# Kernel tuning notes

Measured on AMD Instinct MI355X. Metric: run time of the kernel, lower is better.

Reference implementation:

```python
import jax, jax.numpy as jnp
import numpy as np

B = 4; D = H = W = 28; C = 192; NH = 6; WS = 7; SS = 3
L = D * H * W; N = WS ** 3; HD = C // NH


def _rel_index():
    c = np.stack(np.meshgrid(np.arange(WS), np.arange(WS), np.arange(WS), indexing='ij')).reshape(3, -1)
    r = c[:, :, None] - c[:, None, :] + (WS - 1)
    return jnp.asarray(r[0] * (2 * WS - 1) ** 2 + r[1] * (2 * WS - 1) + r[2])  # (N,N)


def _attn_mask():
    img = np.zeros((D, H, W), np.float32)
    sl = (slice(0, -WS), slice(-WS, -SS), slice(-SS, None))
    cnt = 0
    for d in sl:
        for h in sl:
            for w in sl:
                img[d, h, w] = cnt; cnt += 1
    mw = img.reshape(D // WS, WS, H // WS, WS, W // WS, WS).transpose(0, 2, 4, 1, 3, 5).reshape(-1, N)
    am = mw[:, None, :] - mw[:, :, None]
    return jnp.asarray(np.where(am != 0, -100.0, 0.0).astype(np.float32))  # (nW,N,N)

REL_IDX = _rel_index()
ATTN_MASK = _attn_mask()


def _ln(x, g, b):
    m = x.mean(-1, keepdims=True)
    v = ((x - m) ** 2).mean(-1, keepdims=True)
    return (x - m) / jnp.sqrt(v + 1e-5) * g + b


def _window_partition(x):  # (B,D,H,W,C) -> (B*nW, N, C)
    x = x.reshape(B, D // WS, WS, H // WS, WS, W // WS, WS, C)
    return x.transpose(0, 1, 3, 5, 2, 4, 6, 7).reshape(-1, N, C)


def _window_reverse(w):  # (B*nW, N, C) -> (B,D,H,W,C)
    x = w.reshape(B, D // WS, H // WS, W // WS, WS, WS, WS, C)
    return x.transpose(0, 1, 4, 2, 5, 3, 6, 7).reshape(B, D, H, W, C)


def setup_inputs() -> dict:
    key = jax.random.key(0)
    ks = jax.random.split(key, 8)
    s = 0.02
    return {
        'x': jax.random.normal(ks[0], (B, L, C), jnp.float32),
        'norm1_g': jnp.ones((C,), jnp.float32), 'norm1_b': jnp.zeros((C,), jnp.float32),
        'qkv_w': jax.random.normal(ks[1], (3 * C, C), jnp.float32) * s,
        'qkv_b': jnp.zeros((3 * C,), jnp.float32),
        'proj_w': jax.random.normal(ks[2], (C, C), jnp.float32) * s,
        'proj_b': jnp.zeros((C,), jnp.float32),
        'rel_table': jax.random.normal(ks[3], ((2 * WS - 1) ** 3, NH), jnp.float32) * s,
        'norm2_g': jnp.ones((C,), jnp.float32), 'norm2_b': jnp.zeros((C,), jnp.float32),
        'fc1_w': jax.random.normal(ks[4], (4 * C, C), jnp.float32) * s,
        'fc1_b': jnp.zeros((4 * C,), jnp.float32),
        'fc2_w': jax.random.normal(ks[5], (C, 4 * C), jnp.float32) * s,
        'fc2_b': jnp.zeros((C,), jnp.float32),
    }


def reference(x, norm1_g, norm1_b, qkv_w, qkv_b, proj_w, proj_b, rel_table,
              norm2_g, norm2_b, fc1_w, fc1_b, fc2_w, fc2_b):
    shortcut = x
    h = _ln(x, norm1_g, norm1_b).reshape(B, D, H, W, C)
    h = jnp.roll(h, (-SS, -SS, -SS), axis=(1, 2, 3))
    xw = _window_partition(h)                                  # (B_, N, C)
    B_ = xw.shape[0]
    qkv = (xw @ qkv_w.T + qkv_b).reshape(B_, N, 3, NH, HD).transpose(2, 0, 3, 1, 4)
    q, k, v = qkv[0], qkv[1], qkv[2]                           # (B_, NH, N, HD)
    attn = jnp.einsum('bhnd,bhmd->bhnm', q * (HD ** -0.5), k)
    bias = rel_table[REL_IDX].transpose(2, 0, 1)               # (NH, N, N)
    attn = attn + bias[None]
    nW = ATTN_MASK.shape[0]
    attn = (attn.reshape(B, nW, NH, N, N) + ATTN_MASK[None, :, None]).reshape(B_, NH, N, N)
    attn = jax.nn.softmax(attn, axis=-1)
    out = jnp.einsum('bhnm,bhmd->bhnd', attn, v).transpose(0, 2, 1, 3).reshape(B_, N, C)
    out = out @ proj_w.T + proj_b
    h = _window_reverse(out)
    h = jnp.roll(h, (SS, SS, SS), axis=(1, 2, 3)).reshape(B, L, C)
    x = shortcut + h
    y = _ln(x, norm2_g, norm2_b)
    y = jax.nn.gelu(y @ fc1_w.T + fc1_b, approximate=False)
    return x + (y @ fc2_w.T + fc2_b)
```

## Files before the change

### kernel.cpp

```cpp
#include <hip/hip_runtime.h>

#define DEV __device__ __forceinline__

typedef __bf16 bf16x8 __attribute__((ext_vector_type(8)));
typedef float f32x4 __attribute__((ext_vector_type(4)));

DEV float bflo(unsigned int u) { union { unsigned int x; float f; } c; c.x = u << 16; return c.f; }
DEV unsigned short f2bf(float f) {
  union { float f; unsigned int u; } c; c.f = f;
  unsigned int u = c.u;
  return (unsigned short)((u + 0x7fffu + ((u >> 16) & 1u)) >> 16);
}
DEV unsigned int pkbf(float a, float b) {
  unsigned int r;
  asm("v_cvt_pk_bf16_f32 %0, %1, %2" : "=v"(r) : "v"(a), "v"(b));
  return r;
}
DEV float gelu_fast(float y) {
  float y2 = y * y;
  float z = y * fmaf(y2, 0.10294348f, 2.30220842f);
  float e = __builtin_amdgcn_exp2f(z);
  float r = __builtin_amdgcn_rcpf(e + 1.0f);
  return fmaf(-y, r, y);
}

DEV void gload16(const void* g, void* l) {
  __builtin_amdgcn_global_load_lds((const __attribute__((address_space(1))) void*)g,
                                   (__attribute__((address_space(3))) void*)l, 16, 0, 0);
}

__global__ __launch_bounds__(256) void wconv_all(const float* __restrict__ s0,
                                                 const float* __restrict__ s1,
                                                 const float* __restrict__ s2,
                                                 const float* __restrict__ s3,
                                                 unsigned short* __restrict__ dst) {
  int i = blockIdx.x * 256 + threadIdx.x;
  const float* src; int off, real;
  if (i < 122880)      { src = s0; off = i;          real = 110592; }
  else if (i < 172032) { src = s1; off = i - 122880; real = 36864; }
  else if (i < 319488) { src = s2; off = i - 172032; real = 147456; }
  else                 { src = s3; off = i - 319488; real = 147456; }
  dst[i] = (off < real) ? f2bf(src[off]) : (unsigned short)0;
}

__global__ __launch_bounds__(256) void bmt_kernel(const float* __restrict__ rel_table,
                                                  unsigned short* __restrict__ bmt4) {
  int wth = blockIdx.x;
  int wt = wth / 6, h = wth - wt * 6;
  int r = blockIdx.y;
  unsigned short* row = bmt4 + (((size_t)wth * 88 + r) * 352) * 4;
  for (int q = threadIdx.x; q < 352; q += 256) {
    int mb_q = 0, cls_q = 0;
    bool qv = q < 343;
    if (qv) {
      int ii_q = q / 49, rem_q = q - ii_q * 49;
      int jj_q = rem_q / 7, ww_q = rem_q - jj_q * 7;
      mb_q = ii_q * 169 + jj_q * 13 + ww_q;
      int cd_q = (wt & 4) ? (ii_q < 4 ? 1 : 2) : 0;
      int ch_q = (wt & 2) ? (jj_q < 4 ? 1 : 2) : 0;
      int cw_q = (wt & 1) ? (ww_q < 4 ? 1 : 2) : 0;
      cls_q = cd_q * 9 + ch_q * 3 + cw_q;
    }
    unsigned short ov[4];
#pragma unroll
    for (int i = 0; i < 4; i++) {
      int kk = 4 * r + i;
      float v;
      if (kk >= 343) v = -30000.f;
      else if (!qv) v = 0.f;
      else {
        int ii_k = kk / 49, rem_k = kk - ii_k * 49;
        int jj_k = rem_k / 7, ww_k = rem_k - jj_k * 7;
        int mb_k = ii_k * 169 + jj_k * 13 + ww_k;
        int cd_k = (wt & 4) ? (ii_k < 4 ? 1 : 2) : 0;
        int ch_k = (wt & 2) ? (jj_k < 4 ? 1 : 2) : 0;
        int cw_k = (wt & 1) ? (ww_k < 4 ? 1 : 2) : 0;
        int cls_k = cd_k * 9 + ch_k * 3 + cw_k;
        v = rel_table[(mb_q - mb_k + 1098) * 6 + h] * 1.4426950408889634f;
        if (cls_q != cls_k) v -= 144.26950408889634f;
      }
      ov[i] = f2bf(v);
    }
    unsigned int lo = (unsigned)ov[0] | ((unsigned)ov[1] << 16);
    unsigned int hi = (unsigned)ov[2] | ((unsigned)ov[3] << 16);
    *(uint2*)(row + q * 4) = make_uint2(lo, hi);
  }
}

__global__ __launch_bounds__(256) void ln_kernel(const float* __restrict__ x,
                                                 const float* __restrict__ g,
                                                 const float* __restrict__ b,
                                                 unsigned short* __restrict__ out) {
  int row = (blockIdx.x << 2) + (threadIdx.x >> 6);
  int lane = threadIdx.x & 63;
  int w_ = row / 343, n_ = row - w_ * 343;
  int bb = w_ >> 6, wrem = w_ & 63;
  int wd = wrem >> 4, wh = (wrem >> 2) & 3, ww = wrem & 3;
  int ii = n_ / 49, rem = n_ - ii * 49;
  int jj = rem / 7, kk = rem - jj * 7;
  int d = wd * 7 + ii + 3; if (d >= 28) d -= 28;
  int hh = wh * 7 + jj + 3; if (hh >= 28) hh -= 28;
  int wb = ww * 7 + kk + 3; if (wb >= 28) wb -= 28;
  const float* xr = x + ((size_t)bb * 21952 + (d * 28 + hh) * 28 + wb) * 192;
  float v0 = xr[lane], v1 = xr[lane + 64], v2 = xr[lane + 128];
  float s = v0 + v1 + v2;
  float sq = v0 * v0 + v1 * v1 + v2 * v2;
#pragma unroll
  for (int o = 32; o > 0; o >>= 1) {
    s += __shfl_xor(s, o, 64);
    sq += __shfl_xor(sq, o, 64);
  }
  float mean = s * (1.0f / 192.0f);
  float var = sq * (1.0f / 192.0f) - mean * mean;
  float rstd = rsqrtf(var + 1e-5f);
  unsigned short* orow = out + (size_t)row * 192;
  orow[lane]       = f2bf((v0 - mean) * rstd * g[lane] + b[lane]);
  orow[lane + 64]  = f2bf((v1 - mean) * rstd * g[lane + 64] + b[lane + 64]);
  orow[lane + 128] = f2bf((v2 - mean) * rstd * g[lane + 128] + b[lane + 128]);
}

__global__ __launch_bounds__(256) void gemm_qkv(
    const unsigned short* __restrict__ A, const unsigned short* __restrict__ W,
    const float* __restrict__ bias,
    unsigned short* __restrict__ oq, unsigned short* __restrict__ okk,
    unsigned short* __restrict__ ov) {
  __shared__ __align__(16) unsigned short As[2][128 * 32];
  __shared__ __align__(16) unsigned short Bs[2][128 * 32];
  const int K = 192;
  const int orig = blockIdx.x;
  const int xcd = orig & 7, off = orig >> 3;
  const int wgid = (xcd < 6 ? xcd * 429 : 2574 + (xcd - 6) * 428) + off;
  const int by = wgid / 5, bx = wgid - by * 5;
  const int bm = by << 7, bn = bx << 7;

  const int tid = threadIdx.x;
  const int lane = tid & 63;
  const int wv = tid >> 6;
  const int wr = wv >> 1, wc = wv & 1;
  const int l15 = lane & 15, l4 = lane >> 4;

  f32x4 acc[4][4];
#pragma unroll
  for (int a = 0; a < 4; a++)
#pragma unroll
    for (int b2 = 0; b2 < 4; b2++) acc[a][b2] = (f32x4){0.f, 0.f, 0.f, 0.f};

  auto stage = [&](int kt, int buf) {
#pragma unroll
    for (int i = 0; i < 2; i++) {
      int o = (i << 12) + (tid << 4);
      int r = o >> 6;
      int c = (o >> 4) & 3;
      int sc = (c ^ (r & 3)) << 3;
      gload16(A + (size_t)(bm + r) * K + kt * 32 + sc, &As[buf][o >> 1]);
      gload16(W + (size_t)(bn + r) * K + kt * 32 + sc, &Bs[buf][o >> 1]);
    }
  };

  stage(0, 0);
  int cur = 0;
  for (int kt = 0; kt < 6; ++kt) {
    if (kt < 5) {
      stage(kt + 1, cur ^ 1);
      asm volatile("s_waitcnt vmcnt(4)" ::: "memory");
    } else {
      asm volatile("s_waitcnt vmcnt(0)" ::: "memory");
    }
    __builtin_amdgcn_s_barrier();
    __builtin_amdgcn_sched_barrier(0);
    {
      bf16x8 af[4], bfr[4];
#pragma unroll
      for (int fm = 0; fm < 4; fm++) {
        int r = (wr << 6) + (fm << 4) + l15;
        af[fm] = *(const bf16x8*)(&As[cur][(r << 5) + ((l4 ^ (r & 3)) << 3)]);
      }
#pragma unroll
      for (int fn = 0; fn < 4; fn++) {
        int r = (wc << 6) + (fn << 4) + l15;
        bfr[fn] = *(const bf16x8*)(&Bs[cur][(r << 5) + ((l4 ^ (r & 3)) << 3)]);
      }
#pragma unroll
      for (int fm = 0; fm < 4; fm++)
#pragma unroll
        for (int fn = 0; fn < 4; fn++)
          acc[fm][fn] = __builtin_amdgcn_mfma_f32_16x16x32_bf16(bfr[fn], af[fm], acc[fm][fn], 0, 0, 0);
    }
    if (kt < 5) {
      __builtin_amdgcn_sched_barrier(0);
      __builtin_amdgcn_s_barrier();
      cur ^= 1;
    }
  }

#pragma unroll
  for (int fm = 0; fm < 4; fm++) {
    int gr = bm + (wr << 6) + (fm << 4) + l15;
    int w_ = gr / 343, n_ = gr - w_ * 343;
#pragma unroll
    for (int fn = 0; fn < 4; fn++) {
      int gc0 = bn + (wc << 6) + (fn << 4) + (l4 << 2);
      if (gc0 < 576) {
        float4 bv = *(const float4*)(bias + gc0);
        float v0 = acc[fm][fn][0] + bv.x, v1 = acc[fm][fn][1] + bv.y;
        float v2 = acc[fm][fn][2] + bv.z, v3 = acc[fm][fn][3] + bv.w;
        int which = gc0 / 192;
        int cc3 = gc0 - which * 192;
        int hh2 = cc3 >> 5, dd0 = cc3 & 31;
        size_t offo = ((size_t)(w_ * 6 + hh2) * 343 + n_) * 32 + dd0;
        if (which == 0) {
          const float sc = 0.17677669529663687f * 1.4426950408889634f;
          *(uint2*)(oq + offo) = make_uint2(pkbf(v0 * sc, v1 * sc), pkbf(v2 * sc, v3 * sc));
        } else if (which == 1) {
          *(uint2*)(okk + offo) = make_uint2(pkbf(v0, v1), pkbf(v2, v3));
        } else {
          *(uint2*)(ov + offo) = make_uint2(pkbf(v0, v1), pkbf(v2, v3));
        }
      }
    }
  }
}

__global__ __launch_bounds__(256, 2) void proj_mlp(
    const unsigned short* __restrict__ A,
    const unsigned short* __restrict__ Wp, const float* __restrict__ bp,
    const float* __restrict__ x,
    const float* __restrict__ g2, const float* __restrict__ b2,
    const unsigned short* __restrict__ W1, const float* __restrict__ b1,
    const unsigned short* __restrict__ W2, const float* __restrict__ b2b,
    float* __restrict__ out) {
  __shared__ __align__(16) char smem[41984];
  unsigned short* As = (unsigned short*)smem;
  unsigned short* Hs = (unsigned short*)(smem + 24576);
  float* red = (float*)(smem + 24576);

  const int tid = threadIdx.x, lane = tid & 63, wv = tid >> 6;
  const int l15 = lane & 15, l4 = lane >> 4;
  const int bm = blockIdx.x << 6;

  int orow[4];
#pragma unroll
  for (int fm = 0; fm < 4; fm++) {
    int gr = bm + (fm << 4) + l15;
    int w_ = gr / 343, n_ = gr - w_ * 343;
    int bb = w_ >> 6, wrem = w_ & 63;
    int wd = wrem >> 4, wh = (wrem >> 2) & 3, ww = wrem & 3;
    int ii = n_ / 49, rem = n_ - ii * 49;
    int jj = rem / 7, kk = rem - jj * 7;
    int d = wd * 7 + ii + 3; if (d >= 28) d -= 28;
    int hh = wh * 7 + jj + 3; if (hh >= 28) hh -= 28;
    int wb = ww * 7 + kk + 3; if (wb >= 28) wb -= 28;
    orow[fm] = ((bb * 21952 + (d * 28 + hh) * 28 + wb) * 192);
  }

#pragma unroll
  for (int i = 0; i < 6; i++) {
    int idx = (i << 8) + tid;
    int r = idx / 24, c = idx - r * 24;
    gload16(A + (size_t)(bm + r) * 192 + ((c ^ (r & 7)) << 3), As + r * 192 + (c << 3));
  }
  asm volatile("s_waitcnt vmcnt(0)" ::: "memory");
  __builtin_amdgcn_s_barrier();

  f32x4 acc[4][3];
#pragma unroll
  for (int a = 0; a < 4; a++)
#pragma unroll
    for (int b_ = 0; b_ < 3; b_++) acc[a][b_] = (f32x4){0.f, 0.f, 0.f, 0.f};
  __builtin_amdgcn_s_setprio(1);
#pragma unroll
  for (int ks = 0; ks < 6; ks++) {
    bf16x8 af[4], wpf[3];
#pragma unroll
    for (int fm = 0; fm < 4; fm++) {
      int r = (fm << 4) + l15;
      int ch = (ks << 2) + l4;
      af[fm] = *(const bf16x8*)(As + r * 192 + ((ch ^ (r & 7)) << 3));
    }
#pragma unroll
    for (int fn = 0; fn < 3; fn++) {
      int rr = wv * 48 + (fn << 4) + l15;
      wpf[fn] = *(const bf16x8*)(Wp + (size_t)rr * 192 + (ks << 5) + (l4 << 3));
    }
#pragma unroll
    for (int fm = 0; fm < 4; fm++)
#pragma unroll
      for (int fn = 0; fn < 3; fn++)
        acc[fm][fn] = __builtin_amdgcn_mfma_f32_16x16x32_bf16(wpf[fn], af[fm], acc[fm][fn], 0, 0, 0);
  }
  __builtin_amdgcn_s_setprio(0);

  float ps[4], psq[4];
#pragma unroll
  for (int fm = 0; fm < 4; fm++) {
    float s = 0.f, sq = 0.f;
#pragma unroll
    for (int fn = 0; fn < 3; fn++) {
      int gc0 = wv * 48 + (fn << 4) + (l4 << 2);
      float4 bv = *(const float4*)(bp + gc0);
      float4 xv = *(const float4*)(x + (size_t)orow[fm] + gc0);
      acc[fm][fn][0] += bv.x + xv.x;
      acc[fm][fn][1] += bv.y + xv.y;
      acc[fm][fn][2] += bv.z + xv.z;
      acc[fm][fn][3] += bv.w + xv.w;
#pragma unroll
      for (int i = 0; i < 4; i++) {
        float v = acc[fm][fn][i];
        s += v; sq += v * v;
      }
    }
    ps[fm] = s; psq[fm] = sq;
  }
#pragma unroll
  for (int fm = 0; fm < 4; fm++) {
    ps[fm] += __shfl_xor(ps[fm], 16, 64);
    ps[fm] += __shfl_xor(ps[fm], 32, 64);
    psq[fm] += __shfl_xor(psq[fm], 16, 64);
    psq[fm] += __shfl_xor(psq[fm], 32, 64);
  }
  __syncthreads();
  if (l4 == 0) {
#pragma unroll
    for (int fm = 0; fm < 4; fm++) {
      int tr = (fm << 4) + l15;
      red[tr * 8 + wv] = ps[fm];
      red[tr * 8 + 4 + wv] = psq[fm];
    }
  }
  __syncthreads();
  if (tid < 64) {
    float s = red[tid * 8] + red[tid * 8 + 1] + red[tid * 8 + 2] + red[tid * 8 + 3];
    float sq = red[tid * 8 + 4] + red[tid * 8 + 5] + red[tid * 8 + 6] + red[tid * 8 + 7];
    float mean = s * (1.0f / 192.0f);
    float var = sq * (1.0f / 192.0f) - mean * mean;
    red[tid * 8] = mean;
    red[tid * 8 + 1] = rsqrtf(var + 1e-5f);
  }
  __syncthreads();
  unsigned int xnb[4][3][2];
#pragma unroll
  for (int fm = 0; fm < 4; fm++) {
    int tr = (fm << 4) + l15;
    float mean = red[tr * 8], rstd = red[tr * 8 + 1];
#pragma unroll
    for (int fn = 0; fn < 3; fn++) {
      int gc0 = wv * 48 + (fn << 4) + (l4 << 2);
      float4 gv = *(const float4*)(g2 + gc0);
      float4 b2v = *(const float4*)(b2 + gc0);
      float v0 = acc[fm][fn][0], v1 = acc[fm][fn][1];
      float v2 = acc[fm][fn][2], v3 = acc[fm][fn][3];
      xnb[fm][fn][0] = pkbf(v0, v1);
      xnb[fm][fn][1] = pkbf(v2, v3);
      float y0 = (v0 - mean) * rstd * gv.x + b2v.x;
      float y1 = (v1 - mean) * rstd * gv.y + b2v.y;
      float y2 = (v2 - mean) * rstd * gv.z + b2v.z;
      float y3 = (v3 - mean) * rstd * gv.w + b2v.w;
      int ch = gc0 >> 3;
      *(uint2*)(As + tr * 192 + ((ch ^ (tr & 7)) << 3) + (gc0 & 7)) =
          make_uint2(pkbf(y0, y1), pkbf(y2, y3));
    }
  }
  __syncthreads();

  f32x4 acc2[4][3];
#pragma unroll
  for (int a = 0; a < 4; a++)
#pragma unroll
    for (int b_ = 0; b_ < 3; b_++) acc2[a][b_] = (f32x4){0.f, 0.f, 0.f, 0.f};

#pragma unroll
  for (int cc = 0; cc < 6; cc++) {
    bf16x8 w1f[2][6];
#pragma unroll
    for (int fn = 0; fn < 2; fn++)
#pragma unroll
      for (int ks = 0; ks < 6; ks++) {
        int hrow = (cc << 7) + (wv << 5) + (fn << 4) + l15;
        w1f[fn][ks] = *(const bf16x8*)(W1 + (size_t)hrow * 192 + (ks << 5) + (l4 << 3));
      }
    bf16x8 w2f[3][4];
#pragma unroll
    for (int fn = 0; fn < 3; fn++)
#pragma unroll
      for (int ks = 0; ks < 4; ks++) {
        int j = wv * 48 + (fn << 4) + l15;
        w2f[fn][ks] = *(const bf16x8*)(W2 + (size_t)j * 768 + (cc << 7) + (ks << 5) + (l4 << 3));
      }
    f32x4 acc1[4][2];
#pragma unroll
    for (int a = 0; a < 4; a++) {
      acc1[a][0] = (f32x4){0.f, 0.f, 0.f, 0.f};
      acc1[a][1] = (f32x4){0.f, 0.f, 0.f, 0.f};
    }
    __builtin_amdgcn_s_setprio(1);
#pragma unroll
    for (int ks = 0; ks < 6; ks++) {
      bf16x8 af[4];
#pragma unroll
      for (int fm = 0; fm < 4; fm++) {
        int r = (fm << 4) + l15;
        int ch = (ks << 2) + l4;
        af[fm] = *(const bf16x8*)(As + r * 192 + ((ch ^ (r & 7)) << 3));
      }
#pragma unroll
      for (int fm = 0; fm < 4; fm++)
#pragma unroll
        for (int fn = 0; fn < 2; fn++)
          acc1[fm][fn] = __builtin_amdgcn_mfma_f32_16x16x32_bf16(w1f[fn][ks], af[fm], acc1[fm][fn], 0, 0, 0);
    }
    __builtin_amdgcn_s_setprio(0);
    __syncthreads();
#pragma unroll
    for (int fm = 0; fm < 4; fm++) {
      int r = (fm << 4) + l15;
#pragma unroll
      for (int fn = 0; fn < 2; fn++) {
        int hc = (wv << 5) + (fn << 4) + (l4 << 2);
        float4 bv = *(const float4*)(b1 + (cc << 7) + hc);
        float g0 = gelu_fast(acc1[fm][fn][0] + bv.x);
        float g1 = gelu_fast(acc1[fm][fn][1] + bv.y);
        float g2_ = gelu_fast(acc1[fm][fn][2] + bv.z);
        float g3 = gelu_fast(acc1[fm][fn][3] + bv.w);
        *(uint2*)(Hs + r * 136 + hc) = make_uint2(pkbf(g0, g1), pkbf(g2_, g3));
      }
    }
    __syncthreads();
    __builtin_amdgcn_s_setprio(1);
#pragma unroll
    for (int ks = 0; ks < 4; ks++) {
      bf16x8 hf[4];
#pragma unroll
      for (int fm = 0; fm < 4; fm++) {
        int r = (fm << 4) + l15;
        hf[fm] = *(const bf16x8*)(Hs + r * 136 + (ks << 5) + (l4 << 3));
      }
#pragma unroll
      for (int fm = 0; fm < 4; fm++)
#pragma unroll
        for (int fn = 0; fn < 3; fn++)
          acc2[fm][fn] = __builtin_amdgcn_mfma_f32_16x16x32_bf16(w2f[fn][ks], hf[fm], acc2[fm][fn], 0, 0, 0);
    }
    __builtin_amdgcn_s_setprio(0);
  }

#pragma unroll
  for (int fm = 0; fm < 4; fm++) {
#pragma unroll
    for (int fn = 0; fn < 3; fn++) {
      int gc0 = wv * 48 + (fn << 4) + (l4 << 2);
      float4 bv = *(const float4*)(b2b + gc0);
      float4 o;
      o.x = acc2[fm][fn][0] + bv.x + bflo(xnb[fm][fn][0] & 0xffffu);
      o.y = acc2[fm][fn][1] + bv.y + bflo(xnb[fm][fn][0] >> 16);
      o.z = acc2[fm][fn][2] + bv.z + bflo(xnb[fm][fn][1] & 0xffffu);
      o.w = acc2[fm][fn][3] + bv.w + bflo(xnb[fm][fn][1] >> 16);
      *(float4*)(out + (size_t)orow[fm] + gc0) = o;
    }
  }
}

__global__ __launch_bounds__(256) void attn_mfma(const unsigned short* __restrict__ q,
                                                 const unsigned short* __restrict__ k,
                                                 const unsigned short* __restrict__ v,
                                                 const unsigned short* __restrict__ bmt4,
                                                 unsigned short* __restrict__ out) {
  __shared__ __align__(16) unsigned short Ks[352 * 32];
  __shared__ __align__(16) unsigned short Vt[32 * 360];

  const int blk = blockIdx.x;
  const int h_ = blk >> 8;
  const int idx = blk & 255;
  const int cums[8] = {0, 108, 144, 180, 192, 228, 240, 252};
  int c = (idx >= 108) + (idx >= 144) + (idx >= 180) + (idx >= 192) +
          (idx >= 228) + (idx >= 240) + (idx >= 252);
  int r0 = idx - cums[c];
  int sh = (c & 2) ? 1 : 3, sw = (c & 1) ? 1 : 3;
  int p = ((c & 4) ? 1 : 3) * sh * sw;
  int b = r0 / p, q2 = r0 - b * p;
  int wd, wh, ww;
  if (c & 4) wd = 3; else { wd = q2 / (sh * sw); q2 -= wd * sh * sw; }
  if (c & 2) wh = 3; else { wh = q2 / sw; q2 -= wh * sw; }
  ww = (c & 1) ? 3 : q2;
  const int w_ = b * 64 + wd * 16 + wh * 4 + ww;
  const int wt = c;
  const int blkqkv = w_ * 6 + h_;

  const int t = threadIdx.x, lane = t & 63, wv = t >> 6;
  const int l15 = lane & 15, l4 = lane >> 4;
  const unsigned short* Qb = q + (size_t)blkqkv * (343 * 32);
  const unsigned short* Kb = k + (size_t)blkqkv * (343 * 32);
  const unsigned short* Vb = v + (size_t)blkqkv * (343 * 32);
  const unsigned short* bm4 = bmt4 + ((size_t)(wt * 6 + h_) * 88) * 352 * 4;

  for (int cc = t; cc < 1408; cc += 256) {
    int r = cc >> 2, ch = cc & 3;
    int swc = ch ^ ((r >> 1) & 3);
    uint4 val = make_uint4(0, 0, 0, 0);
    if (r < 343) val = *(const uint4*)(Kb + r * 32 + ch * 8);
    *(uint4*)(Ks + r * 32 + swc * 8) = val;
  }
#pragma unroll
  for (int ch = 0; ch < 4; ch++) {
    for (int n = t; n < 343; n += 256) {
      union { uint4 u4; unsigned short us[8]; } val;
      val.u4 = *(const uint4*)(Vb + n * 32 + ch * 8);
#pragma unroll
      for (int j = 0; j < 8; j++) Vt[(ch * 8 + j) * 360 + n] = val.us[j];
    }
  }
  for (int cc = t; cc < 288; cc += 256) {
    int d = cc / 9, n = 343 + (cc - d * 9);
    Vt[d * 360 + n] = 0;
  }
  __syncthreads();

  const int ksw = (l4 ^ ((l15 >> 1) & 3)) << 3;

  for (int tq = wv; tq < 22; tq += 4) {
    int qrow = tq * 16 + l15; if (qrow > 342) qrow = 342;
    bf16x8 qf = *(const bf16x8*)(Qb + qrow * 32 + l4 * 8);

    unsigned int u0[22], u1[22];
    float lsum = 0.f;
    __builtin_amdgcn_s_setprio(1);
#pragma unroll
    for (int kt = 0; kt < 22; kt++) {
      bf16x8 kf = *(const bf16x8*)(Ks + (kt * 16 + l15) * 32 + ksw);
      f32x4 s = __builtin_amdgcn_mfma_f32_16x16x32_bf16(kf, qf, (f32x4){0.f, 0.f, 0.f, 0.f}, 0, 0, 0);
      const unsigned short* bp = bm4 + ((size_t)((kt << 2) + l4) * 352 + (tq << 4) + l15) * 4;
      uint2 bv = *(const uint2*)bp;
      float p0 = __builtin_amdgcn_exp2f(s[0] + bflo(bv.x & 0xffffu));
      float p1 = __builtin_amdgcn_exp2f(s[1] + bflo(bv.x >> 16));
      float p2 = __builtin_amdgcn_exp2f(s[2] + bflo(bv.y & 0xffffu));
      float p3 = __builtin_amdgcn_exp2f(s[3] + bflo(bv.y >> 16));
      lsum += (p0 + p1) + (p2 + p3);
      asm("v_cvt_pk_bf16_f32 %0, %1, %2" : "=v"(u0[kt]) : "v"(p0), "v"(p1));
      asm("v_cvt_pk_bf16_f32 %0, %1, %2" : "=v"(u1[kt]) : "v"(p2), "v"(p3));
    }
    __builtin_amdgcn_s_setprio(0);
    lsum += __shfl_xor(lsum, 16, 64);
    lsum += __shfl_xor(lsum, 32, 64);
    float inv = 1.0f / lsum;

    f32x4 oacc0 = (f32x4){0.f, 0.f, 0.f, 0.f};
    f32x4 oacc1 = (f32x4){0.f, 0.f, 0.f, 0.f};
    __builtin_amdgcn_s_setprio(1);
#pragma unroll
    for (int ck = 0; ck < 11; ck++) {
      unsigned int dw[4];
#pragma unroll
      for (int d = 0; d < 4; d++) {
        int src = l15 + 16 * ((d >> 1) + 2 * (l4 & 1));
        unsigned int x = __shfl((d & 1) ? u1[2 * ck] : u0[2 * ck], src, 64);
        unsigned int y = __shfl((d & 1) ? u1[2 * ck + 1] : u0[2 * ck + 1], src, 64);
        dw[d] = (l4 < 2) ? x : y;
      }
      union { unsigned int u[4]; bf16x8 v; } pc;
      pc.u[0] = dw[0]; pc.u[1] = dw[1]; pc.u[2] = dw[2]; pc.u[3] = dw[3];
      bf16x8 vf0 = *(const bf16x8*)(Vt + (size_t)l15 * 360 + ck * 32 + l4 * 8);
      bf16x8 vf1 = *(const bf16x8*)(Vt + (size_t)(16 + l15) * 360 + ck * 32 + l4 * 8);
      oacc0 = __builtin_amdgcn_mfma_f32_16x16x32_bf16(vf0, pc.v, oacc0, 0, 0, 0);
      oacc1 = __builtin_amdgcn_mfma_f32_16x16x32_bf16(vf1, pc.v, oacc1, 0, 0, 0);
    }
    __builtin_amdgcn_s_setprio(0);

    int qg = tq * 16 + l15;
    if (qg < 343) {
      unsigned short* orow = out + ((size_t)w_ * 343 + qg) * 192 + h_ * 32;
      *(uint2*)(orow + (l4 << 2)) =
          make_uint2(pkbf(oacc0[0] * inv, oacc0[1] * inv), pkbf(oacc0[2] * inv, oacc0[3] * inv));
      *(uint2*)(orow + 16 + (l4 << 2)) =
          make_uint2(pkbf(oacc1[0] * inv, oacc1[1] * inv), pkbf(oacc1[2] * inv, oacc1[3] * inv));
    }
  }
}

extern "C" void kernel_launch(void* const* d_in, const int* in_sizes, int n_in,
                              void* d_out, int out_size, void* d_ws, size_t ws_size,
                              hipStream_t stream) {
  const float* x      = (const float*)d_in[0];
  const float* n1g    = (const float*)d_in[1];
  const float* n1b    = (const float*)d_in[2];
  const float* qkv_w  = (const float*)d_in[3];
  const float* qkv_b  = (const float*)d_in[4];
  const float* proj_w = (const float*)d_in[5];
  const float* proj_b = (const float*)d_in[6];
  const float* rel_t  = (const float*)d_in[7];
  const float* n2g    = (const float*)d_in[8];
  const float* n2b    = (const float*)d_in[9];
  const float* fc1_w  = (const float*)d_in[10];
  const float* fc1_b  = (const float*)d_in[11];
  const float* fc2_w  = (const float*)d_in[12];
  const float* fc2_b  = (const float*)d_in[13];

  char* ws = (char*)d_ws;
  if (ws_size < 147820032ull) return;
  unsigned short* WQKV  = (unsigned short*)(ws);
  unsigned short* WPROJ = (unsigned short*)(ws + 245760);
  unsigned short* WFC1  = (unsigned short*)(ws + 344064);
  unsigned short* WFC2  = (unsigned short*)(ws + 638976);
  unsigned short* XW    = (unsigned short*)(ws + 1032192);
  unsigned short* Q_    = (unsigned short*)(ws + 34750464);
  unsigned short* K_    = (unsigned short*)(ws + 68468736);
  unsigned short* V_    = (unsigned short*)(ws + 102187008);
  unsigned short* BMT4  = (unsigned short*)(ws + 135925248);
  float* OUT = (float*)d_out;

  wconv_all<<<2016, 256, 0, stream>>>(qkv_w, proj_w, fc1_w, fc2_w, WQKV);

  bmt_kernel<<<dim3(48, 88), 256, 0, stream>>>(rel_t, BMT4);

  ln_kernel<<<21952, 256, 0, stream>>>(x, n1g, n1b, XW);

  gemm_qkv<<<3430, 256, 0, stream>>>(XW, WQKV, qkv_b, Q_, K_, V_);

  attn_mfma<<<1536, 256, 0, stream>>>(Q_, K_, V_, BMT4, XW);

  proj_mlp<<<1372, 256, 0, stream>>>(XW, WPROJ, proj_b, x, n2g, n2b,
                                     WFC1, fc1_b, WFC2, fc2_b, OUT);
}
```

Baseline: 324.1 us.

## Widen proj_mlp blocks to 128 rows with double-buffered GELU tile

The fused proj+LN+MLP kernel now uses 512-thread blocks that cover 128 rows, in two row groups of four waves. Each weight fragment the kernel loads therefore feeds twice as many rows, halving the block count. The hidden (GELU) tile is double-buffered so the barrier before writing it can be dropped, and the W2 fragment loads move after the fc1 MFMAs to shorten their live range. The s_setprio hints are removed. In exchange, LDS per block rises to about 116 KB, which likely allows only one block per CU, and the tighter register budget may cause spills or lower occupancy.

```diff
diff --git a/kernel.cpp b/kernel.cpp
--- a/kernel.cpp
+++ b/kernel.cpp
@@ -221,7 +221,7 @@
   }
 }
 
-__global__ __launch_bounds__(256, 2) void proj_mlp(
+__global__ __launch_bounds__(512, 2) void proj_mlp(
     const unsigned short* __restrict__ A,
     const unsigned short* __restrict__ Wp, const float* __restrict__ bp,
     const float* __restrict__ x,
@@ -229,19 +229,21 @@
     const unsigned short* __restrict__ W1, const float* __restrict__ b1,
     const unsigned short* __restrict__ W2, const float* __restrict__ b2b,
     float* __restrict__ out) {
-  __shared__ __align__(16) char smem[41984];
-  unsigned short* As = (unsigned short*)smem;
-  unsigned short* Hs = (unsigned short*)(smem + 24576);
-  float* red = (float*)(smem + 24576);
+  __shared__ __align__(16) char smem[118784];
+  unsigned short* As  = (unsigned short*)smem;
+  unsigned short* Hs0 = (unsigned short*)(smem + 49152);
+  unsigned short* Hs1 = (unsigned short*)(smem + 83968);
+  float* red = (float*)(smem + 49152);
 
   const int tid = threadIdx.x, lane = tid & 63, wv = tid >> 6;
+  const int wq = wv & 3, rg = wv >> 2;
   const int l15 = lane & 15, l4 = lane >> 4;
-  const int bm = blockIdx.x << 6;
+  const int bm = blockIdx.x << 7;
 
   int orow[4];
 #pragma unroll
   for (int fm = 0; fm < 4; fm++) {
-    int gr = bm + (fm << 4) + l15;
+    int gr = bm + (rg << 6) + (fm << 4) + l15;
     int w_ = gr / 343, n_ = gr - w_ * 343;
     int bb = w_ >> 6, wrem = w_ & 63;
     int wd = wrem >> 4, wh = (wrem >> 2) & 3, ww = wrem & 3;
@@ -255,7 +257,7 @@
 
 #pragma unroll
   for (int i = 0; i < 6; i++) {
-    int idx = (i << 8) + tid;
+    int idx = (i << 9) + tid;
     int r = idx / 24, c = idx - r * 24;
     gload16(A + (size_t)(bm + r) * 192 + ((c ^ (r & 7)) << 3), As + r * 192 + (c << 3));
   }
@@ -267,19 +269,18 @@
   for (int a = 0; a < 4; a++)
 #pragma unroll
     for (int b_ = 0; b_ < 3; b_++) acc[a][b_] = (f32x4){0.f, 0.f, 0.f, 0.f};
-  __builtin_amdgcn_s_setprio(1);
 #pragma unroll
   for (int ks = 0; ks < 6; ks++) {
     bf16x8 af[4], wpf[3];
 #pragma unroll
     for (int fm = 0; fm < 4; fm++) {
-      int r = (fm << 4) + l15;
+      int r = (rg << 6) + (fm << 4) + l15;
       int ch = (ks << 2) + l4;
       af[fm] = *(const bf16x8*)(As + r * 192 + ((ch ^ (r & 7)) << 3));
     }
 #pragma unroll
     for (int fn = 0; fn < 3; fn++) {
-      int rr = wv * 48 + (fn << 4) + l15;
+      int rr = wq * 48 + (fn << 4) + l15;
       wpf[fn] = *(const bf16x8*)(Wp + (size_t)rr * 192 + (ks << 5) + (l4 << 3));
     }
 #pragma unroll
@@ -288,7 +289,6 @@
       for (int fn = 0; fn < 3; fn++)
         acc[fm][fn] = __builtin_amdgcn_mfma_f32_16x16x32_bf16(wpf[fn], af[fm], acc[fm][fn], 0, 0, 0);
   }
-  __builtin_amdgcn_s_setprio(0);
 
   float ps[4], psq[4];
 #pragma unroll
@@ -296,7 +296,7 @@
     float s = 0.f, sq = 0.f;
 #pragma unroll
     for (int fn = 0; fn < 3; fn++) {
-      int gc0 = wv * 48 + (fn << 4) + (l4 << 2);
+      int gc0 = wq * 48 + (fn << 4) + (l4 << 2);
       float4 bv = *(const float4*)(bp + gc0);
       float4 xv = *(const float4*)(x + (size_t)orow[fm] + gc0);
       acc[fm][fn][0] += bv.x + xv.x;
@@ -322,13 +322,13 @@
   if (l4 == 0) {
 #pragma unroll
     for (int fm = 0; fm < 4; fm++) {
-      int tr = (fm << 4) + l15;
-      red[tr * 8 + wv] = ps[fm];
-      red[tr * 8 + 4 + wv] = psq[fm];
+      int tr = (rg << 6) + (fm << 4) + l15;
+      red[tr * 8 + wq] = ps[fm];
+      red[tr * 8 + 4 + wq] = psq[fm];
     }
   }
   __syncthreads();
-  if (tid < 64) {
+  if (tid < 128) {
     float s = red[tid * 8] + red[tid * 8 + 1] + red[tid * 8 + 2] + red[tid * 8 + 3];
     float sq = red[tid * 8 + 4] + red[tid * 8 + 5] + red[tid * 8 + 6] + red[tid * 8 + 7];
     float mean = s * (1.0f / 192.0f);
@@ -340,11 +340,11 @@
   unsigned int xnb[4][3][2];
 #pragma unroll
   for (int fm = 0; fm < 4; fm++) {
-    int tr = (fm << 4) + l15;
+    int tr = (rg << 6) + (fm << 4) + l15;
     float mean = red[tr * 8], rstd = red[tr * 8 + 1];
 #pragma unroll
     for (int fn = 0; fn < 3; fn++) {
-      int gc0 = wv * 48 + (fn << 4) + (l4 << 2);
+      int gc0 = wq * 48 + (fn << 4) + (l4 << 2);
       float4 gv = *(const float4*)(g2 + gc0);
       float4 b2v = *(const float4*)(b2 + gc0);
       float v0 = acc[fm][fn][0], v1 = acc[fm][fn][1];
@@ -370,21 +370,14 @@
 
 #pragma unroll
   for (int cc = 0; cc < 6; cc++) {
+    unsigned short* Hc = (cc & 1) ? Hs1 : Hs0;
     bf16x8 w1f[2][6];
 #pragma unroll
     for (int fn = 0; fn < 2; fn++)
 #pragma unroll
       for (int ks = 0; ks < 6; ks++) {
-        int hrow = (cc << 7) + (wv << 5) + (fn << 4) + l15;
+        int hrow = (cc << 7) + (wq << 5) + (fn << 4) + l15;
         w1f[fn][ks] = *(const bf16x8*)(W1 + (size_t)hrow * 192 + (ks << 5) + (l4 << 3));
-      }
-    bf16x8 w2f[3][4];
-#pragma unroll
-    for (int fn = 0; fn < 3; fn++)
-#pragma unroll
-      for (int ks = 0; ks < 4; ks++) {
-        int j = wv * 48 + (fn << 4) + l15;
-        w2f[fn][ks] = *(const bf16x8*)(W2 + (size_t)j * 768 + (cc << 7) + (ks << 5) + (l4 << 3));
       }
     f32x4 acc1[4][2];
 #pragma unroll
@@ -392,13 +385,12 @@
       acc1[a][0] = (f32x4){0.f, 0.f, 0.f, 0.f};
       acc1[a][1] = (f32x4){0.f, 0.f, 0.f, 0.f};
     }
-    __builtin_amdgcn_s_setprio(1);
 #pragma unroll
     for (int ks = 0; ks < 6; ks++) {
       bf16x8 af[4];
 #pragma unroll
       for (int fm = 0; fm < 4; fm++) {
-        int r = (fm << 4) + l15;
+        int r = (rg << 6) + (fm << 4) + l15;
         int ch = (ks << 2) + l4;
         af[fm] = *(const bf16x8*)(As + r * 192 + ((ch ^ (r & 7)) << 3));
       }
@@ -408,31 +400,36 @@
         for (int fn = 0; fn < 2; fn++)
           acc1[fm][fn] = __builtin_amdgcn_mfma_f32_16x16x32_bf16(w1f[fn][ks], af[fm], acc1[fm][fn], 0, 0, 0);
     }
-    __builtin_amdgcn_s_setprio(0);
-    __syncthreads();
+    bf16x8 w2f[3][4];
+#pragma unroll
+    for (int fn = 0; fn < 3; fn++)
+#pragma unroll
+      for (int ks = 0; ks < 4; ks++) {
+        int j = wq * 48 + (fn << 4) + l15;
+        w2f[fn][ks] = *(const bf16x8*)(W2 + (size_t)j * 768 + (cc << 7) + (ks << 5) + (l4 << 3));
+      }
 #pragma unroll
     for (int fm = 0; fm < 4; fm++) {
-      int r = (fm << 4) + l15;
+      int r = (rg << 6) + (fm << 4) + l15;
 #pragma unroll
       for (int fn = 0; fn < 2; fn++) {
-        int hc = (wv << 5) + (fn << 4) + (l4 << 2);
+        int hc = (wq << 5) + (fn << 4) + (l4 << 2);
         float4 bv = *(const float4*)(b1 + (cc << 7) + hc);
         float g0 = gelu_fast(acc1[fm][fn][0] + bv.x);
         float g1 = gelu_fast(acc1[fm][fn][1] + bv.y);
         float g2_ = gelu_fast(acc1[fm][fn][2] + bv.z);
         float g3 = gelu_fast(acc1[fm][fn][3] + bv.w);
-        *(uint2*)(Hs + r * 136 + hc) = make_uint2(pkbf(g0, g1), pkbf(g2_, g3));
+        *(uint2*)(Hc + r * 136 + hc) = make_uint2(pkbf(g0, g1), pkbf(g2_, g3));
       }
     }
     __syncthreads();
-    __builtin_amdgcn_s_setprio(1);
 #pragma unroll
     for (int ks = 0; ks < 4; ks++) {
       bf16x8 hf[4];
 #pragma unroll
       for (int fm = 0; fm < 4; fm++) {
-        int r = (fm << 4) + l15;
-        hf[fm] = *(const bf16x8*)(Hs + r * 136 + (ks << 5) + (l4 << 3));
+        int r = (rg << 6) + (fm << 4) + l15;
+        hf[fm] = *(const bf16x8*)(Hc + r * 136 + (ks << 5) + (l4 << 3));
       }
 #pragma unroll
       for (int fm = 0; fm < 4; fm++)
@@ -440,14 +437,13 @@
         for (int fn = 0; fn < 3; fn++)
           acc2[fm][fn] = __builtin_amdgcn_mfma_f32_16x16x32_bf16(w2f[fn][ks], hf[fm], acc2[fm][fn], 0, 0, 0);
     }
-    __builtin_amdgcn_s_setprio(0);
   }
 
 #pragma unroll
   for (int fm = 0; fm < 4; fm++) {
 #pragma unroll
     for (int fn = 0; fn < 3; fn++) {
-      int gc0 = wv * 48 + (fn << 4) + (l4 << 2);
+      int gc0 = wq * 48 + (fn << 4) + (l4 << 2);
       float4 bv = *(const float4*)(b2b + gc0);
       float4 o;
       o.x = acc2[fm][fn][0] + bv.x + bflo(xnb[fm][fn][0] & 0xffffu);
@@ -616,6 +612,6 @@
 
   attn_mfma<<<1536, 256, 0, stream>>>(Q_, K_, V_, BMT4, XW);
 
-  proj_mlp<<<1372, 256, 0, stream>>>(XW, WPROJ, proj_b, x, n2g, n2b,
-                                     WFC1, fc1_b, WFC2, fc2_b, OUT);
-}
+  proj_mlp<<<686, 512, 0, stream>>>(XW, WPROJ, proj_b, x, n2g, n2b,
+                                    WFC1, fc1_b, WFC2, fc2_b, OUT);
+}
```

Result: no change. 323.7 us (-0.1%).
